# Kernel optimization log

Measured on AMD Instinct MI355X. Metric: run time of the kernel, lower is better.

The kernel has to match this reference:

```python
import jax, jax.numpy as jnp
import numpy as np

GROUP = 64   # quantization group size (nunchaku W4A4 default)
QMAX = 7.0   # symmetric int4 positive range


def setup_inputs() -> dict:
    key = jax.random.key(0)
    ks = jax.random.split(key, 6)
    T, K, N, R = 256, 3072, 3072, 32
    x = jax.random.normal(ks[0], (T, K), dtype=jnp.float32)
    # int4 weight codes stored as 0..15 (dequant subtracts zero-point 8)
    qweight = jax.random.randint(ks[1], (N, K), 0, 16, dtype=jnp.int32)
    # per-(out_channel, input_group) weight scales, small positive
    wscales = jax.random.uniform(ks[2], (N, K // GROUP), dtype=jnp.float32) * 0.02 + 1e-3
    lora_down = jax.random.normal(ks[3], (R, K), dtype=jnp.float32) / np.sqrt(K)
    lora_up = jax.random.normal(ks[4], (N, R), dtype=jnp.float32) / np.sqrt(R)
    bias = jax.random.normal(ks[5], (N,), dtype=jnp.float32) * 0.01
    return {"x": x, "qweight": qweight, "wscales": wscales,
            "lora_down": lora_down, "lora_up": lora_up, "bias": bias}


def _quantize_act(x):
    # per-token, per-group symmetric int4 fake-quant (quantize -> dequantize)
    T, K = x.shape
    xg = x.reshape(T, K // GROUP, GROUP)
    scale = jnp.maximum(jnp.max(jnp.abs(xg), axis=-1, keepdims=True) / QMAX, 1e-8)
    q = jnp.clip(jnp.round(xg / scale), -8.0, QMAX)
    return (q * scale).reshape(T, K)


def reference(x, qweight, wscales, lora_down, lora_up, bias):
    # Dequantize int4 weights: (code - 8) * per-group scale  -> [N, K]
    N, K = qweight.shape
    w = (qweight.astype(jnp.float32) - 8.0).reshape(N, K // GROUP, GROUP)
    w = (w * wscales[:, :, None]).reshape(N, K)
    # W4A4 main path: int4-quantized activations x dequantized int4 weights
    x_dq = _quantize_act(x)
    main = x_dq @ w.T                               # [T, N]
    # fused low-rank (SVDQuant LoRA) branch on full-precision activations
    lora = (x @ lora_down.T) @ lora_up.T            # [T, R] @ [R, N]
    return main + lora + bias
```

## Files before the change

kernel.cpp:

```cpp
#include <hip/hip_runtime.h>
#include <stdint.h>

#define T_DIM 256
#define K_DIM 3072
#define N_DIM 3072
#define R_DIM 32
#define KG    48
#define NSPLIT 6

#define PQ_BLOCKS 4608
#define QA_BLOCKS 3072
#define LM_BLOCKS 96
#define BO_BLOCKS 768

typedef __bf16 bf16x8 __attribute__((ext_vector_type(8)));
typedef float  f32x4  __attribute__((ext_vector_type(4)));
typedef unsigned short u16x8 __attribute__((ext_vector_type(8)));

__device__ __forceinline__ unsigned short f2bf(float f) {
    unsigned u = __builtin_bit_cast(unsigned, f);
    unsigned rounding = 0x7FFFu + ((u >> 16) & 1u);
    return (unsigned short)((u + rounding) >> 16);
}

__device__ __forceinline__ bf16x8 cvt8(const float* p) {
    float4 lo = ((const float4*)p)[0], hi = ((const float4*)p)[1];
    bf16x8 v;
    v[0] = (__bf16)lo.x; v[1] = (__bf16)lo.y; v[2] = (__bf16)lo.z; v[3] = (__bf16)lo.w;
    v[4] = (__bf16)hi.x; v[5] = (__bf16)hi.y; v[6] = (__bf16)hi.z; v[7] = (__bf16)hi.w;
    return v;
}

__global__ __launch_bounds__(256) void prep(
        const int*   __restrict__ qweight,
        const float* __restrict__ x,
        const float* __restrict__ lora_down,
        const float* __restrict__ bias,
        unsigned*       __restrict__ Qp,
        unsigned short* __restrict__ Ap,
        float*          __restrict__ Lm,
        float*          __restrict__ out) {
    int blk = blockIdx.x;
    if (blk < PQ_BLOCKS) {
        size_t o = (size_t)blk * 256 + threadIdx.x;
        unsigned kt  = (unsigned)(o / 24576u);
        unsigned rem = (unsigned)(o % 24576u);
        unsigned n = rem >> 3, wi = rem & 7;
        const int4* p = (const int4*)(qweight + (size_t)n * K_DIM + (size_t)kt * 64 + wi * 8);
        int4 a = p[0], b = p[1];
        unsigned w = (unsigned)(a.x & 15)        | ((unsigned)(a.y & 15) << 4)
                   | ((unsigned)(a.z & 15) << 8) | ((unsigned)(a.w & 15) << 12)
                   | ((unsigned)(b.x & 15) << 16)| ((unsigned)(b.y & 15) << 20)
                   | ((unsigned)(b.z & 15) << 24)| ((unsigned)(b.w & 15) << 28);
        Qp[o] = w;
    } else if (blk < PQ_BLOCKS + QA_BLOCKS) {
        int widx = (blk - PQ_BLOCKS) * 4 + (threadIdx.x >> 6);
        int lane = threadIdx.x & 63;
        int t = widx / KG, g = widx % KG;
        float v = x[(size_t)t * K_DIM + g * 64 + lane];
        float a = fabsf(v);
        #pragma unroll
        for (int off = 32; off; off >>= 1) a = fmaxf(a, __shfl_xor(a, off));
        float scale = fmaxf(a / 7.0f, 1e-8f);
        float q = rintf(v / scale);
        q = fminf(fmaxf(q, -8.f), 7.f);
        Ap[(((size_t)g * 8 + (lane >> 3)) * 256 + t) * 8 + (lane & 7)] = f2bf(q * scale);
    } else if (blk < PQ_BLOCKS + QA_BLOCKS + LM_BLOCKS) {
        int kb = blk - PQ_BLOCKS - QA_BLOCKS;
        int lane = threadIdx.x & 63, wv = threadIdx.x >> 6;
        int mrow = lane & 15, quad = lane >> 4;
        int k0 = kb * 32 + quad * 8;
        bf16x8 a[4], b[2];
        #pragma unroll
        for (int mt = 0; mt < 4; ++mt)
            a[mt] = cvt8(x + (size_t)(wv * 64 + mt * 16 + mrow) * K_DIM + k0);
        #pragma unroll
        for (int nt = 0; nt < 2; ++nt)
            b[nt] = cvt8(lora_down + (size_t)(nt * 16 + mrow) * K_DIM + k0);
        f32x4 acc[4][2];
        f32x4 zero = {0.f, 0.f, 0.f, 0.f};
        #pragma unroll
        for (int i = 0; i < 4; ++i) { acc[i][0] = zero; acc[i][1] = zero; }
        #pragma unroll
        for (int mt = 0; mt < 4; ++mt)
            #pragma unroll
            for (int nt = 0; nt < 2; ++nt)
                acc[mt][nt] = __builtin_amdgcn_mfma_f32_16x16x32_bf16(
                    a[mt], b[nt], acc[mt][nt], 0, 0, 0);
        #pragma unroll
        for (int mt = 0; mt < 4; ++mt)
            #pragma unroll
            for (int nt = 0; nt < 2; ++nt)
                #pragma unroll
                for (int r = 0; r < 4; ++r)
                    atomicAdd(&Lm[(size_t)(wv * 64 + mt * 16 + quad * 4 + r) * R_DIM
                                  + nt * 16 + mrow], acc[mt][nt][r]);
    } else {
        int i = (blk - PQ_BLOCKS - QA_BLOCKS - LM_BLOCKS) * 256 + threadIdx.x;
        float4 bv = *(const float4*)&bias[(i * 4) % N_DIM];
        ((float4*)out)[i] = bv;
    }
}

__global__ __launch_bounds__(256) void gemm_main(
        const uint4*    __restrict__ ApU,
        const unsigned* __restrict__ Qp,
        const float*    __restrict__ wscales,
        const float*    __restrict__ Lm,
        const float*    __restrict__ lora_up,
        float*          __restrict__ out) {
    __shared__ uint4 BsU[2][512];
    int nblk  = blockIdx.x;
    int mblk  = blockIdx.y;
    int split = blockIdx.z;
    int c0 = split * (KG / NSPLIT);
    int c1 = (split == NSPLIT - 1) ? KG + 1 : c0 + (KG / NSPLIT);
    int tid = threadIdx.x;
    int lane = tid & 63, wv = tid >> 6;
    int mrow = lane & 15, quad = lane >> 4;
    int n_row = tid >> 2, seg = tid & 3;
    const int nbase = nblk * 64;
    const int mbase = mblk * 128 + wv * 32;

    f32x4 acc[2][4];
    f32x4 zero = {0.f, 0.f, 0.f, 0.f};
    #pragma unroll
    for (int i = 0; i < 2; ++i)
        #pragma unroll
        for (int j = 0; j < 4; ++j) acc[i][j] = zero;

    uint2 ubc[2];
    float wsr[2];
    bf16x8 af[2][2][2];

    const float* wsrow = wscales + (size_t)(nbase + n_row) * KG;

    #define AFRAG(kt, ks, mt) \
        (*(const bf16x8*)&ApU[(size_t)(kt) * 2048 + ((ks) * 4 + quad) * 256 + \
                              mbase + (mt) * 16 + mrow])

    {
        #pragma unroll
        for (int ks = 0; ks < 2; ++ks)
            #pragma unroll
            for (int mt = 0; mt < 2; ++mt)
                af[0][ks][mt] = AFRAG(c0, ks, mt);
        const unsigned* q0 = Qp + ((size_t)c0 * N_DIM + nbase + n_row) * 8 + seg * 2;
        const unsigned* q1 = Qp + ((size_t)(c0 + 1) * N_DIM + nbase + n_row) * 8 + seg * 2;
        ubc[0] = *(const uint2*)q0;
        ubc[1] = *(const uint2*)q1;
        wsr[0] = wsrow[c0];
        wsr[1] = wsrow[c0 + 1];
    }

    #define STEP(PP, KT)                                                          \
    {                                                                             \
        constexpr int p = (PP);                                                   \
        const int kk = (KT);                                                      \
        if (kk < KG) {                                                            \
            float w = wsr[p];                                                     \
            float m8w = -8.0f * w;                                                \
            unsigned u0 = ubc[p].x, u1 = ubc[p].y;                                \
            unsigned e0 = u0 & 0x0F0F0F0Fu, od0 = (u0 >> 4) & 0x0F0F0F0Fu;        \
            unsigned e1 = u1 & 0x0F0F0F0Fu, od1 = (u1 >> 4) & 0x0F0F0F0Fu;        \
            bf16x8 v0, v1;                                                        \
            _Pragma("unroll")                                                     \
            for (int j = 0; j < 4; ++j) {                                         \
                v0[2*j]   = (__bf16)__builtin_fmaf((float)((e0  >> (8*j)) & 0xFFu), w, m8w); \
                v0[2*j+1] = (__bf16)__builtin_fmaf((float)((od0 >> (8*j)) & 0xFFu), w, m8w); \
                v1[2*j]   = (__bf16)__builtin_fmaf((float)((e1  >> (8*j)) & 0xFFu), w, m8w); \
                v1[2*j+1] = (__bf16)__builtin_fmaf((float)((od1 >> (8*j)) & 0xFFu), w, m8w); \
            }                                                                     \
            BsU[p][(seg * 2 + 0) * 64 + n_row] = __builtin_bit_cast(uint4, v0);   \
            BsU[p][(seg * 2 + 1) * 64 + n_row] = __builtin_bit_cast(uint4, v1);   \
        } else {                                                                  \
            bf16x8 v0 = __builtin_bit_cast(bf16x8, (u16x8)(0));                   \
            bf16x8 v1 = __builtin_bit_cast(bf16x8, (u16x8)(0));                   \
            if (seg < 2) {                                                        \
                const float* lu = lora_up + (size_t)(nbase + n_row) * R_DIM + seg * 16; \
                _Pragma("unroll")                                                 \
                for (int j = 0; j < 8; ++j) {                                     \
                    v0[j] = (__bf16)lu[j];                                        \
                    v1[j] = (__bf16)lu[8 + j];                                    \
                }                                                                 \
            }                                                                     \
            BsU[p][(seg * 2 + 0) * 64 + n_row] = __builtin_bit_cast(uint4, v0);   \
            BsU[p][(seg * 2 + 1) * 64 + n_row] = __builtin_bit_cast(uint4, v1);   \
        }                                                                         \
        __syncthreads();                                                          \
        if (kk + 2 < c1 && kk + 2 < KG) {                                         \
            const unsigned* q2 = Qp + ((size_t)(kk + 2) * N_DIM + nbase + n_row) * 8 + seg * 2; \
            ubc[p] = *(const uint2*)q2;                                           \
            wsr[p] = wsrow[kk + 2];                                               \
        }                                                                         \
        if (kk + 1 < c1) {                                                        \
            if (kk + 1 < KG) {                                                    \
                _Pragma("unroll")                                                 \
                for (int ks = 0; ks < 2; ++ks)                                    \
                    _Pragma("unroll")                                             \
                    for (int mt = 0; mt < 2; ++mt)                                \
                        af[p ^ 1][ks][mt] = AFRAG(kk + 1, ks, mt);                \
            } else {                                                              \
                _Pragma("unroll")                                                 \
                for (int mt = 0; mt < 2; ++mt) {                                  \
                    int row = mbase + mt * 16 + mrow;                             \
                    if (quad < 4)                                                 \
                        af[p ^ 1][0][mt] = cvt8(Lm + (size_t)row * R_DIM + quad * 8); \
                    else                                                          \
                        af[p ^ 1][0][mt] = __builtin_bit_cast(bf16x8, (u16x8)(0)); \
                    af[p ^ 1][1][mt] = __builtin_bit_cast(bf16x8, (u16x8)(0));    \
                }                                                                 \
            }                                                                     \
        }                                                                         \
        _Pragma("unroll")                                                         \
        for (int ks = 0; ks < 2; ++ks) {                                          \
            bf16x8 b[4];                                                          \
            _Pragma("unroll")                                                     \
            for (int nt = 0; nt < 4; ++nt) {                                      \
                uint4 tb = BsU[p][(ks * 4 + quad) * 64 + nt * 16 + mrow];         \
                b[nt] = __builtin_bit_cast(bf16x8, tb);                           \
            }                                                                     \
            _Pragma("unroll")                                                     \
            for (int mt = 0; mt < 2; ++mt)                                        \
                _Pragma("unroll")                                                 \
                for (int nt = 0; nt < 4; ++nt)                                    \
                    acc[mt][nt] = __builtin_amdgcn_mfma_f32_16x16x32_bf16(        \
                        af[p][ks][mt], b[nt], acc[mt][nt], 0, 0, 0);              \
        }                                                                         \
    }

    int kt = c0;
    for (; kt + 1 < c1; kt += 2) {
        STEP(0, kt);
        STEP(1, kt + 1);
    }
    if (kt < c1) STEP(0, kt);

    #undef STEP
    #undef AFRAG
    #pragma unroll
    for (int nt = 0; nt < 4; ++nt) {
        int n = nbase + nt * 16 + mrow;
        #pragma unroll
        for (int mt = 0; mt < 2; ++mt) {
            int row0 = mblk * 128 + wv * 32 + mt * 16 + quad * 4;
            #pragma unroll
            for (int r = 0; r < 4; ++r)
                atomicAdd(&out[(size_t)(row0 + r) * N_DIM + n], acc[mt][nt][r]);
        }
    }
}

extern "C" void kernel_launch(void* const* d_in, const int* in_sizes, int n_in,
                              void* d_out, int out_size, void* d_ws, size_t ws_size,
                              hipStream_t stream) {
    const float* x         = (const float*)d_in[0];
    const int*   qweight   = (const int*)d_in[1];
    const float* wscales   = (const float*)d_in[2];
    const float* lora_down = (const float*)d_in[3];
    const float* lora_up   = (const float*)d_in[4];
    const float* bias      = (const float*)d_in[5];

    char* wsp = (char*)d_ws;
    unsigned short* Ap = (unsigned short*)wsp;
    wsp += (size_t)KG * 2048 * 16;
    float* Lm = (float*)wsp;
    wsp += (size_t)T_DIM * R_DIM * 4;
    unsigned* Qp = (unsigned*)wsp;

    hipMemsetAsync(Lm, 0, (size_t)T_DIM * R_DIM * sizeof(float), stream);
    prep<<<PQ_BLOCKS + QA_BLOCKS + LM_BLOCKS + BO_BLOCKS, 256, 0, stream>>>(
        qweight, x, lora_down, bias, Qp, Ap, Lm, (float*)d_out);
    gemm_main<<<dim3(48, 2, NSPLIT), 256, 0, stream>>>(
        (const uint4*)Ap, Qp, wscales, Lm, lora_up, (float*)d_out);
}
```

Before: 119.3 us.

## Fuse prep and GEMM into one persistent kernel with grid barriers

Merges the prep kernel (weight packing, activation quantization, bias init, LoRA-down) and the main GEMM into a single 576-block launch. Grid-wide spin barriers separate the phases, and the prep work is spread across blocks with strided loops. The Lm memset is folded into the kernel, so only a small barrier memset is still launched. This removes a kernel launch and the inter-kernel gap, but the barrier only works if all 576 blocks are co-resident, and it has a timeout escape that could silently break ordering.

```diff
diff --git a/kernel.cpp b/kernel.cpp
--- a/kernel.cpp
+++ b/kernel.cpp
@@ -8,10 +8,7 @@
 #define KG    48
 #define NSPLIT 6
 
-#define PQ_BLOCKS 4608
-#define QA_BLOCKS 3072
-#define LM_BLOCKS 96
-#define BO_BLOCKS 768
+#define GRID_BLOCKS 576
 
 typedef __bf16 bf16x8 __attribute__((ext_vector_type(8)));
 typedef float  f32x4  __attribute__((ext_vector_type(4)));
@@ -31,43 +28,80 @@
     return v;
 }
 
-__global__ __launch_bounds__(256) void prep(
+__device__ __forceinline__ void grid_barrier(unsigned* cell) {
+    __syncthreads();
+    if (threadIdx.x == 0) {
+        __hip_atomic_fetch_add(cell, 1u, __ATOMIC_RELEASE, __HIP_MEMORY_SCOPE_AGENT);
+        unsigned long long t0 = __builtin_amdgcn_s_memrealtime();
+        while (__hip_atomic_load(cell, __ATOMIC_ACQUIRE, __HIP_MEMORY_SCOPE_AGENT)
+               < (unsigned)GRID_BLOCKS) {
+            __builtin_amdgcn_s_sleep(8);
+            if (__builtin_amdgcn_s_memrealtime() - t0 > (1ULL << 24)) break;
+        }
+    }
+    __syncthreads();
+}
+
+__global__ __launch_bounds__(256, 3) void fused(
+        const float* __restrict__ x,
         const int*   __restrict__ qweight,
-        const float* __restrict__ x,
+        const float* __restrict__ wscales,
         const float* __restrict__ lora_down,
+        const float* __restrict__ lora_up,
         const float* __restrict__ bias,
         unsigned*       __restrict__ Qp,
         unsigned short* __restrict__ Ap,
         float*          __restrict__ Lm,
+        unsigned*       __restrict__ bar,
         float*          __restrict__ out) {
-    int blk = blockIdx.x;
-    if (blk < PQ_BLOCKS) {
-        size_t o = (size_t)blk * 256 + threadIdx.x;
-        unsigned kt  = (unsigned)(o / 24576u);
-        unsigned rem = (unsigned)(o % 24576u);
-        unsigned n = rem >> 3, wi = rem & 7;
-        const int4* p = (const int4*)(qweight + (size_t)n * K_DIM + (size_t)kt * 64 + wi * 8);
-        int4 a = p[0], b = p[1];
-        unsigned w = (unsigned)(a.x & 15)        | ((unsigned)(a.y & 15) << 4)
-                   | ((unsigned)(a.z & 15) << 8) | ((unsigned)(a.w & 15) << 12)
-                   | ((unsigned)(b.x & 15) << 16)| ((unsigned)(b.y & 15) << 20)
-                   | ((unsigned)(b.z & 15) << 24)| ((unsigned)(b.w & 15) << 28);
-        Qp[o] = w;
-    } else if (blk < PQ_BLOCKS + QA_BLOCKS) {
-        int widx = (blk - PQ_BLOCKS) * 4 + (threadIdx.x >> 6);
-        int lane = threadIdx.x & 63;
-        int t = widx / KG, g = widx % KG;
-        float v = x[(size_t)t * K_DIM + g * 64 + lane];
-        float a = fabsf(v);
-        #pragma unroll
-        for (int off = 32; off; off >>= 1) a = fmaxf(a, __shfl_xor(a, off));
-        float scale = fmaxf(a / 7.0f, 1e-8f);
-        float q = rintf(v / scale);
-        q = fminf(fmaxf(q, -8.f), 7.f);
-        Ap[(((size_t)g * 8 + (lane >> 3)) * 256 + t) * 8 + (lane & 7)] = f2bf(q * scale);
-    } else if (blk < PQ_BLOCKS + QA_BLOCKS + LM_BLOCKS) {
-        int kb = blk - PQ_BLOCKS - QA_BLOCKS;
-        int lane = threadIdx.x & 63, wv = threadIdx.x >> 6;
+    __shared__ uint4 BsU[2][512];
+    const int blk = blockIdx.x;
+    const int tid = threadIdx.x;
+
+    {
+        #pragma unroll
+        for (int i = 0; i < 8; ++i) {
+            size_t o = ((size_t)blk * 8 + i) * 256 + tid;
+            unsigned kt  = (unsigned)(o / 24576u);
+            unsigned rem = (unsigned)(o % 24576u);
+            unsigned n = rem >> 3, wi = rem & 7;
+            const int4* p = (const int4*)(qweight + (size_t)n * K_DIM + (size_t)kt * 64 + wi * 8);
+            int4 a = p[0], b = p[1];
+            unsigned w = (unsigned)(a.x & 15)        | ((unsigned)(a.y & 15) << 4)
+                       | ((unsigned)(a.z & 15) << 8) | ((unsigned)(a.w & 15) << 12)
+                       | ((unsigned)(b.x & 15) << 16)| ((unsigned)(b.y & 15) << 20)
+                       | ((unsigned)(b.z & 15) << 24)| ((unsigned)(b.w & 15) << 28);
+            Qp[o] = w;
+        }
+    }
+    {
+        int lane = tid & 63;
+        int wgl  = blk * 4 + (tid >> 6);
+        for (int u = wgl; u < T_DIM * KG; u += GRID_BLOCKS * 4) {
+            int t = u / KG, g = u % KG;
+            float v = x[(size_t)t * K_DIM + g * 64 + lane];
+            float a = fabsf(v);
+            #pragma unroll
+            for (int off = 32; off; off >>= 1) a = fmaxf(a, __shfl_xor(a, off));
+            float scale = fmaxf(a / 7.0f, 1e-8f);
+            float q = rintf(v / scale);
+            q = fminf(fmaxf(q, -8.f), 7.f);
+            Ap[(((size_t)g * 8 + (lane >> 3)) * 256 + t) * 8 + (lane & 7)] = f2bf(q * scale);
+        }
+    }
+    {
+        for (int u = blk * 256 + tid; u < T_DIM * N_DIM / 4; u += GRID_BLOCKS * 256) {
+            float4 bv = *(const float4*)&bias[(u * 4) % N_DIM];
+            ((float4*)out)[u] = bv;
+        }
+    }
+    if (blk < 32) Lm[blk * 256 + tid] = 0.f;
+
+    grid_barrier(&bar[0]);
+
+    if (blk < 96) {
+        int kb = blk;
+        int lane = tid & 63, wv = tid >> 6;
         int mrow = lane & 15, quad = lane >> 4;
         int k0 = kb * 32 + quad * 8;
         bf16x8 a[4], b[2];
@@ -95,158 +129,151 @@
                 for (int r = 0; r < 4; ++r)
                     atomicAdd(&Lm[(size_t)(wv * 64 + mt * 16 + quad * 4 + r) * R_DIM
                                   + nt * 16 + mrow], acc[mt][nt][r]);
-    } else {
-        int i = (blk - PQ_BLOCKS - QA_BLOCKS - LM_BLOCKS) * 256 + threadIdx.x;
-        float4 bv = *(const float4*)&bias[(i * 4) % N_DIM];
-        ((float4*)out)[i] = bv;
-    }
-}
-
-__global__ __launch_bounds__(256) void gemm_main(
-        const uint4*    __restrict__ ApU,
-        const unsigned* __restrict__ Qp,
-        const float*    __restrict__ wscales,
-        const float*    __restrict__ Lm,
-        const float*    __restrict__ lora_up,
-        float*          __restrict__ out) {
-    __shared__ uint4 BsU[2][512];
-    int nblk  = blockIdx.x;
-    int mblk  = blockIdx.y;
-    int split = blockIdx.z;
-    int c0 = split * (KG / NSPLIT);
-    int c1 = (split == NSPLIT - 1) ? KG + 1 : c0 + (KG / NSPLIT);
-    int tid = threadIdx.x;
-    int lane = tid & 63, wv = tid >> 6;
-    int mrow = lane & 15, quad = lane >> 4;
-    int n_row = tid >> 2, seg = tid & 3;
-    const int nbase = nblk * 64;
-    const int mbase = mblk * 128 + wv * 32;
-
-    f32x4 acc[2][4];
-    f32x4 zero = {0.f, 0.f, 0.f, 0.f};
-    #pragma unroll
-    for (int i = 0; i < 2; ++i)
-        #pragma unroll
-        for (int j = 0; j < 4; ++j) acc[i][j] = zero;
-
-    uint2 ubc[2];
-    float wsr[2];
-    bf16x8 af[2][2][2];
-
-    const float* wsrow = wscales + (size_t)(nbase + n_row) * KG;
-
-    #define AFRAG(kt, ks, mt) \
-        (*(const bf16x8*)&ApU[(size_t)(kt) * 2048 + ((ks) * 4 + quad) * 256 + \
-                              mbase + (mt) * 16 + mrow])
+    }
+
+    grid_barrier(&bar[1]);
 
     {
-        #pragma unroll
-        for (int ks = 0; ks < 2; ++ks)
-            #pragma unroll
-            for (int mt = 0; mt < 2; ++mt)
-                af[0][ks][mt] = AFRAG(c0, ks, mt);
-        const unsigned* q0 = Qp + ((size_t)c0 * N_DIM + nbase + n_row) * 8 + seg * 2;
-        const unsigned* q1 = Qp + ((size_t)(c0 + 1) * N_DIM + nbase + n_row) * 8 + seg * 2;
-        ubc[0] = *(const uint2*)q0;
-        ubc[1] = *(const uint2*)q1;
-        wsr[0] = wsrow[c0];
-        wsr[1] = wsrow[c0 + 1];
-    }
-
-    #define STEP(PP, KT)                                                          \
-    {                                                                             \
-        constexpr int p = (PP);                                                   \
-        const int kk = (KT);                                                      \
-        if (kk < KG) {                                                            \
-            float w = wsr[p];                                                     \
-            float m8w = -8.0f * w;                                                \
-            unsigned u0 = ubc[p].x, u1 = ubc[p].y;                                \
-            unsigned e0 = u0 & 0x0F0F0F0Fu, od0 = (u0 >> 4) & 0x0F0F0F0Fu;        \
-            unsigned e1 = u1 & 0x0F0F0F0Fu, od1 = (u1 >> 4) & 0x0F0F0F0Fu;        \
-            bf16x8 v0, v1;                                                        \
-            _Pragma("unroll")                                                     \
-            for (int j = 0; j < 4; ++j) {                                         \
-                v0[2*j]   = (__bf16)__builtin_fmaf((float)((e0  >> (8*j)) & 0xFFu), w, m8w); \
-                v0[2*j+1] = (__bf16)__builtin_fmaf((float)((od0 >> (8*j)) & 0xFFu), w, m8w); \
-                v1[2*j]   = (__bf16)__builtin_fmaf((float)((e1  >> (8*j)) & 0xFFu), w, m8w); \
-                v1[2*j+1] = (__bf16)__builtin_fmaf((float)((od1 >> (8*j)) & 0xFFu), w, m8w); \
-            }                                                                     \
-            BsU[p][(seg * 2 + 0) * 64 + n_row] = __builtin_bit_cast(uint4, v0);   \
-            BsU[p][(seg * 2 + 1) * 64 + n_row] = __builtin_bit_cast(uint4, v1);   \
-        } else {                                                                  \
-            bf16x8 v0 = __builtin_bit_cast(bf16x8, (u16x8)(0));                   \
-            bf16x8 v1 = __builtin_bit_cast(bf16x8, (u16x8)(0));                   \
-            if (seg < 2) {                                                        \
-                const float* lu = lora_up + (size_t)(nbase + n_row) * R_DIM + seg * 16; \
-                _Pragma("unroll")                                                 \
-                for (int j = 0; j < 8; ++j) {                                     \
-                    v0[j] = (__bf16)lu[j];                                        \
-                    v1[j] = (__bf16)lu[8 + j];                                    \
-                }                                                                 \
-            }                                                                     \
-            BsU[p][(seg * 2 + 0) * 64 + n_row] = __builtin_bit_cast(uint4, v0);   \
-            BsU[p][(seg * 2 + 1) * 64 + n_row] = __builtin_bit_cast(uint4, v1);   \
-        }                                                                         \
-        __syncthreads();                                                          \
-        if (kk + 2 < c1 && kk + 2 < KG) {                                         \
-            const unsigned* q2 = Qp + ((size_t)(kk + 2) * N_DIM + nbase + n_row) * 8 + seg * 2; \
-            ubc[p] = *(const uint2*)q2;                                           \
-            wsr[p] = wsrow[kk + 2];                                               \
-        }                                                                         \
-        if (kk + 1 < c1) {                                                        \
-            if (kk + 1 < KG) {                                                    \
-                _Pragma("unroll")                                                 \
-                for (int ks = 0; ks < 2; ++ks)                                    \
-                    _Pragma("unroll")                                             \
-                    for (int mt = 0; mt < 2; ++mt)                                \
-                        af[p ^ 1][ks][mt] = AFRAG(kk + 1, ks, mt);                \
-            } else {                                                              \
-                _Pragma("unroll")                                                 \
-                for (int mt = 0; mt < 2; ++mt) {                                  \
-                    int row = mbase + mt * 16 + mrow;                             \
-                    if (quad < 4)                                                 \
-                        af[p ^ 1][0][mt] = cvt8(Lm + (size_t)row * R_DIM + quad * 8); \
-                    else                                                          \
-                        af[p ^ 1][0][mt] = __builtin_bit_cast(bf16x8, (u16x8)(0)); \
-                    af[p ^ 1][1][mt] = __builtin_bit_cast(bf16x8, (u16x8)(0));    \
-                }                                                                 \
-            }                                                                     \
-        }                                                                         \
-        _Pragma("unroll")                                                         \
-        for (int ks = 0; ks < 2; ++ks) {                                          \
-            bf16x8 b[4];                                                          \
-            _Pragma("unroll")                                                     \
-            for (int nt = 0; nt < 4; ++nt) {                                      \
-                uint4 tb = BsU[p][(ks * 4 + quad) * 64 + nt * 16 + mrow];         \
-                b[nt] = __builtin_bit_cast(bf16x8, tb);                           \
-            }                                                                     \
-            _Pragma("unroll")                                                     \
-            for (int mt = 0; mt < 2; ++mt)                                        \
-                _Pragma("unroll")                                                 \
-                for (int nt = 0; nt < 4; ++nt)                                    \
-                    acc[mt][nt] = __builtin_amdgcn_mfma_f32_16x16x32_bf16(        \
-                        af[p][ks][mt], b[nt], acc[mt][nt], 0, 0, 0);              \
-        }                                                                         \
-    }
-
-    int kt = c0;
-    for (; kt + 1 < c1; kt += 2) {
-        STEP(0, kt);
-        STEP(1, kt + 1);
-    }
-    if (kt < c1) STEP(0, kt);
-
-    #undef STEP
-    #undef AFRAG
-    #pragma unroll
-    for (int nt = 0; nt < 4; ++nt) {
-        int n = nbase + nt * 16 + mrow;
-        #pragma unroll
-        for (int mt = 0; mt < 2; ++mt) {
-            int row0 = mblk * 128 + wv * 32 + mt * 16 + quad * 4;
-            #pragma unroll
-            for (int r = 0; r < 4; ++r)
-                atomicAdd(&out[(size_t)(row0 + r) * N_DIM + n], acc[mt][nt][r]);
+        const uint4* ApU = (const uint4*)Ap;
+        int split = blk / 96;
+        int rem   = blk % 96;
+        int nblk  = rem % 48;
+        int mblk  = rem / 48;
+        int c0 = split * (KG / NSPLIT);
+        int c1 = (split == NSPLIT - 1) ? KG + 1 : c0 + (KG / NSPLIT);
+        int lane = tid & 63, wv = tid >> 6;
+        int mrow = lane & 15, quad = lane >> 4;
+        int n_row = tid >> 2, seg = tid & 3;
+        const int nbase = nblk * 64;
+        const int mbase = mblk * 128 + wv * 32;
+
+        f32x4 acc[2][4];
+        f32x4 zero = {0.f, 0.f, 0.f, 0.f};
+        #pragma unroll
+        for (int i = 0; i < 2; ++i)
+            #pragma unroll
+            for (int j = 0; j < 4; ++j) acc[i][j] = zero;
+
+        uint2 ubc[2];
+        float wsr[2];
+        bf16x8 af[2][2][2];
+
+        const float* wsrow = wscales + (size_t)(nbase + n_row) * KG;
+
+        #define AFRAG(kt, ks, mt) \
+            (*(const bf16x8*)&ApU[(size_t)(kt) * 2048 + ((ks) * 4 + quad) * 256 + \
+                                  mbase + (mt) * 16 + mrow])
+
+        {
+            #pragma unroll
+            for (int ks = 0; ks < 2; ++ks)
+                #pragma unroll
+                for (int mt = 0; mt < 2; ++mt)
+                    af[0][ks][mt] = AFRAG(c0, ks, mt);
+            const unsigned* q0 = Qp + ((size_t)c0 * N_DIM + nbase + n_row) * 8 + seg * 2;
+            const unsigned* q1 = Qp + ((size_t)(c0 + 1) * N_DIM + nbase + n_row) * 8 + seg * 2;
+            ubc[0] = *(const uint2*)q0;
+            ubc[1] = *(const uint2*)q1;
+            wsr[0] = wsrow[c0];
+            wsr[1] = wsrow[c0 + 1];
+        }
+
+        #define STEP(PP, KT)                                                          \
+        {                                                                             \
+            constexpr int p = (PP);                                                   \
+            const int kk = (KT);                                                      \
+            if (kk < KG) {                                                            \
+                float w = wsr[p];                                                     \
+                float m8w = -8.0f * w;                                                \
+                unsigned u0 = ubc[p].x, u1 = ubc[p].y;                                \
+                unsigned e0 = u0 & 0x0F0F0F0Fu, od0 = (u0 >> 4) & 0x0F0F0F0Fu;        \
+                unsigned e1 = u1 & 0x0F0F0F0Fu, od1 = (u1 >> 4) & 0x0F0F0F0Fu;        \
+                bf16x8 v0, v1;                                                        \
+                _Pragma("unroll")                                                     \
+                for (int j = 0; j < 4; ++j) {                                         \
+                    v0[2*j]   = (__bf16)__builtin_fmaf((float)((e0  >> (8*j)) & 0xFFu), w, m8w); \
+                    v0[2*j+1] = (__bf16)__builtin_fmaf((float)((od0 >> (8*j)) & 0xFFu), w, m8w); \
+                    v1[2*j]   = (__bf16)__builtin_fmaf((float)((e1  >> (8*j)) & 0xFFu), w, m8w); \
+                    v1[2*j+1] = (__bf16)__builtin_fmaf((float)((od1 >> (8*j)) & 0xFFu), w, m8w); \
+                }                                                                     \
+                BsU[p][(seg * 2 + 0) * 64 + n_row] = __builtin_bit_cast(uint4, v0);   \
+                BsU[p][(seg * 2 + 1) * 64 + n_row] = __builtin_bit_cast(uint4, v1);   \
+            } else {                                                                  \
+                bf16x8 v0 = __builtin_bit_cast(bf16x8, (u16x8)(0));                   \
+                bf16x8 v1 = __builtin_bit_cast(bf16x8, (u16x8)(0));                   \
+                if (seg < 2) {                                                        \
+                    const float* lu = lora_up + (size_t)(nbase + n_row) * R_DIM + seg * 16; \
+                    _Pragma("unroll")                                                 \
+                    for (int j = 0; j < 8; ++j) {                                     \
+                        v0[j] = (__bf16)lu[j];                                        \
+                        v1[j] = (__bf16)lu[8 + j];                                    \
+                    }                                                                 \
+                }                                                                     \
+                BsU[p][(seg * 2 + 0) * 64 + n_row] = __builtin_bit_cast(uint4, v0);   \
+                BsU[p][(seg * 2 + 1) * 64 + n_row] = __builtin_bit_cast(uint4, v1);   \
+            }                                                                         \
+            __syncthreads();                                                          \
+            if (kk + 2 < c1 && kk + 2 < KG) {                                         \
+                const unsigned* q2 = Qp + ((size_t)(kk + 2) * N_DIM + nbase + n_row) * 8 + seg * 2; \
+                ubc[p] = *(const uint2*)q2;                                           \
+                wsr[p] = wsrow[kk + 2];                                               \
+            }                                                                         \
+            if (kk + 1 < c1) {                                                        \
+                if (kk + 1 < KG) {                                                    \
+                    _Pragma("unroll")                                                 \
+                    for (int ks = 0; ks < 2; ++ks)                                    \
+                        _Pragma("unroll")                                             \
+                        for (int mt = 0; mt < 2; ++mt)                                \
+                            af[p ^ 1][ks][mt] = AFRAG(kk + 1, ks, mt);                \
+                } else {                                                              \
+                    _Pragma("unroll")                                                 \
+                    for (int mt = 0; mt < 2; ++mt) {                                  \
+                        int row = mbase + mt * 16 + mrow;                             \
+                        if (quad < 4)                                                 \
+                            af[p ^ 1][0][mt] = cvt8(Lm + (size_t)row * R_DIM + quad * 8); \
+                        else                                                          \
+                            af[p ^ 1][0][mt] = __builtin_bit_cast(bf16x8, (u16x8)(0)); \
+                        af[p ^ 1][1][mt] = __builtin_bit_cast(bf16x8, (u16x8)(0));    \
+                    }                                                                 \
+                }                                                                     \
+            }                                                                         \
+            _Pragma("unroll")                                                         \
+            for (int ks = 0; ks < 2; ++ks) {                                          \
+                bf16x8 b[4];                                                          \
+                _Pragma("unroll")                                                     \
+                for (int nt = 0; nt < 4; ++nt) {                                      \
+                    uint4 tb = BsU[p][(ks * 4 + quad) * 64 + nt * 16 + mrow];         \
+                    b[nt] = __builtin_bit_cast(bf16x8, tb);                           \
+                }                                                                     \
+                _Pragma("unroll")                                                     \
+                for (int mt = 0; mt < 2; ++mt)                                        \
+                    _Pragma("unroll")                                                 \
+                    for (int nt = 0; nt < 4; ++nt)                                    \
+                        acc[mt][nt] = __builtin_amdgcn_mfma_f32_16x16x32_bf16(        \
+                            af[p][ks][mt], b[nt], acc[mt][nt], 0, 0, 0);              \
+            }                                                                         \
+        }
+
+        int kt = c0;
+        for (; kt + 1 < c1; kt += 2) {
+            STEP(0, kt);
+            STEP(1, kt + 1);
+        }
+        if (kt < c1) STEP(0, kt);
+
+        #undef STEP
+        #undef AFRAG
+
+        #pragma unroll
+        for (int nt = 0; nt < 4; ++nt) {
+            int n = nbase + nt * 16 + mrow;
+            #pragma unroll
+            for (int mt = 0; mt < 2; ++mt) {
+                int row0 = mblk * 128 + wv * 32 + mt * 16 + quad * 4;
+                #pragma unroll
+                for (int r = 0; r < 4; ++r)
+                    atomicAdd(&out[(size_t)(row0 + r) * N_DIM + n], acc[mt][nt][r]);
+            }
         }
     }
 }
@@ -267,10 +294,11 @@
     float* Lm = (float*)wsp;
     wsp += (size_t)T_DIM * R_DIM * 4;
     unsigned* Qp = (unsigned*)wsp;
-
-    hipMemsetAsync(Lm, 0, (size_t)T_DIM * R_DIM * sizeof(float), stream);
-    prep<<<PQ_BLOCKS + QA_BLOCKS + LM_BLOCKS + BO_BLOCKS, 256, 0, stream>>>(
-        qweight, x, lora_down, bias, Qp, Ap, Lm, (float*)d_out);
-    gemm_main<<<dim3(48, 2, NSPLIT), 256, 0, stream>>>(
-        (const uint4*)Ap, Qp, wscales, Lm, lora_up, (float*)d_out);
-}
+    wsp += (size_t)N_DIM * (K_DIM / 8) * 4;
+    unsigned* bar = (unsigned*)wsp;
+
+    hipMemsetAsync(bar, 0, 64, stream);
+    fused<<<GRID_BLOCKS, 256, 0, stream>>>(
+        x, qweight, wscales, lora_down, lora_up, bias,
+        Qp, Ap, Lm, bar, (float*)d_out);
+}
```

Measured after the change: 252.8 us. 2.12x slower.

## Dequantize raw int32 weight codes directly in GEMM, dropping the nibble-packing pre-pass

Applied to the files above, without the earlier changes.

The prep kernel no longer repacks int32 weight codes into 4-bit nibbles in a workspace buffer. The main GEMM now loads the raw int32 codes straight from qweight (four int4 vectors per thread per k-tile), converts each code to float and applies the group scale while staging into shared memory. This removes one full pass over the weights and the write-then-read of the packed buffer. In exchange, the GEMM streams the full 32-bit codes, and each weight row is fetched by both M blocks. It also holds many more registers for the prefetched codes, which may lower occupancy.

```diff
diff --git a/kernel.cpp b/kernel.cpp
--- a/kernel.cpp
+++ b/kernel.cpp
@@ -8,7 +8,6 @@
 #define KG    48
 #define NSPLIT 6
 
-#define PQ_BLOCKS 4608
 #define QA_BLOCKS 3072
 #define LM_BLOCKS 96
 #define BO_BLOCKS 768
@@ -32,29 +31,15 @@
 }
 
 __global__ __launch_bounds__(256) void prep(
-        const int*   __restrict__ qweight,
         const float* __restrict__ x,
         const float* __restrict__ lora_down,
         const float* __restrict__ bias,
-        unsigned*       __restrict__ Qp,
         unsigned short* __restrict__ Ap,
         float*          __restrict__ Lm,
         float*          __restrict__ out) {
     int blk = blockIdx.x;
-    if (blk < PQ_BLOCKS) {
-        size_t o = (size_t)blk * 256 + threadIdx.x;
-        unsigned kt  = (unsigned)(o / 24576u);
-        unsigned rem = (unsigned)(o % 24576u);
-        unsigned n = rem >> 3, wi = rem & 7;
-        const int4* p = (const int4*)(qweight + (size_t)n * K_DIM + (size_t)kt * 64 + wi * 8);
-        int4 a = p[0], b = p[1];
-        unsigned w = (unsigned)(a.x & 15)        | ((unsigned)(a.y & 15) << 4)
-                   | ((unsigned)(a.z & 15) << 8) | ((unsigned)(a.w & 15) << 12)
-                   | ((unsigned)(b.x & 15) << 16)| ((unsigned)(b.y & 15) << 20)
-                   | ((unsigned)(b.z & 15) << 24)| ((unsigned)(b.w & 15) << 28);
-        Qp[o] = w;
-    } else if (blk < PQ_BLOCKS + QA_BLOCKS) {
-        int widx = (blk - PQ_BLOCKS) * 4 + (threadIdx.x >> 6);
+    if (blk < QA_BLOCKS) {
+        int widx = blk * 4 + (threadIdx.x >> 6);
         int lane = threadIdx.x & 63;
         int t = widx / KG, g = widx % KG;
         float v = x[(size_t)t * K_DIM + g * 64 + lane];
@@ -65,8 +50,8 @@
         float q = rintf(v / scale);
         q = fminf(fmaxf(q, -8.f), 7.f);
         Ap[(((size_t)g * 8 + (lane >> 3)) * 256 + t) * 8 + (lane & 7)] = f2bf(q * scale);
-    } else if (blk < PQ_BLOCKS + QA_BLOCKS + LM_BLOCKS) {
-        int kb = blk - PQ_BLOCKS - QA_BLOCKS;
+    } else if (blk < QA_BLOCKS + LM_BLOCKS) {
+        int kb = blk - QA_BLOCKS;
         int lane = threadIdx.x & 63, wv = threadIdx.x >> 6;
         int mrow = lane & 15, quad = lane >> 4;
         int k0 = kb * 32 + quad * 8;
@@ -96,7 +81,7 @@
                     atomicAdd(&Lm[(size_t)(wv * 64 + mt * 16 + quad * 4 + r) * R_DIM
                                   + nt * 16 + mrow], acc[mt][nt][r]);
     } else {
-        int i = (blk - PQ_BLOCKS - QA_BLOCKS - LM_BLOCKS) * 256 + threadIdx.x;
+        int i = (blk - QA_BLOCKS - LM_BLOCKS) * 256 + threadIdx.x;
         float4 bv = *(const float4*)&bias[(i * 4) % N_DIM];
         ((float4*)out)[i] = bv;
     }
@@ -104,7 +89,7 @@
 
 __global__ __launch_bounds__(256) void gemm_main(
         const uint4*    __restrict__ ApU,
-        const unsigned* __restrict__ Qp,
+        const int*      __restrict__ qweight,
         const float*    __restrict__ wscales,
         const float*    __restrict__ Lm,
         const float*    __restrict__ lora_up,
@@ -129,11 +114,12 @@
         #pragma unroll
         for (int j = 0; j < 4; ++j) acc[i][j] = zero;
 
-    uint2 ubc[2];
+    int4  qc[2][4];
     float wsr[2];
     bf16x8 af[2][2][2];
 
     const float* wsrow = wscales + (size_t)(nbase + n_row) * KG;
+    const int4* qrow = (const int4*)(qweight + (size_t)(nbase + n_row) * K_DIM + seg * 16);
 
     #define AFRAG(kt, ks, mt) \
         (*(const bf16x8*)&ApU[(size_t)(kt) * 2048 + ((ks) * 4 + quad) * 256 + \
@@ -145,10 +131,11 @@
             #pragma unroll
             for (int mt = 0; mt < 2; ++mt)
                 af[0][ks][mt] = AFRAG(c0, ks, mt);
-        const unsigned* q0 = Qp + ((size_t)c0 * N_DIM + nbase + n_row) * 8 + seg * 2;
-        const unsigned* q1 = Qp + ((size_t)(c0 + 1) * N_DIM + nbase + n_row) * 8 + seg * 2;
-        ubc[0] = *(const uint2*)q0;
-        ubc[1] = *(const uint2*)q1;
+        #pragma unroll
+        for (int j = 0; j < 4; ++j) {
+            qc[0][j] = qrow[(size_t)c0 * 16 + j];
+            qc[1][j] = qrow[(size_t)(c0 + 1) * 16 + j];
+        }
         wsr[0] = wsrow[c0];
         wsr[1] = wsrow[c0 + 1];
     }
@@ -160,17 +147,24 @@
         if (kk < KG) {                                                            \
             float w = wsr[p];                                                     \
             float m8w = -8.0f * w;                                                \
-            unsigned u0 = ubc[p].x, u1 = ubc[p].y;                                \
-            unsigned e0 = u0 & 0x0F0F0F0Fu, od0 = (u0 >> 4) & 0x0F0F0F0Fu;        \
-            unsigned e1 = u1 & 0x0F0F0F0Fu, od1 = (u1 >> 4) & 0x0F0F0F0Fu;        \
+            int4 ca = qc[p][0], cb = qc[p][1], cc = qc[p][2], cd = qc[p][3];      \
             bf16x8 v0, v1;                                                        \
-            _Pragma("unroll")                                                     \
-            for (int j = 0; j < 4; ++j) {                                         \
-                v0[2*j]   = (__bf16)__builtin_fmaf((float)((e0  >> (8*j)) & 0xFFu), w, m8w); \
-                v0[2*j+1] = (__bf16)__builtin_fmaf((float)((od0 >> (8*j)) & 0xFFu), w, m8w); \
-                v1[2*j]   = (__bf16)__builtin_fmaf((float)((e1  >> (8*j)) & 0xFFu), w, m8w); \
-                v1[2*j+1] = (__bf16)__builtin_fmaf((float)((od1 >> (8*j)) & 0xFFu), w, m8w); \
-            }                                                                     \
+            v0[0] = (__bf16)__builtin_fmaf((float)ca.x, w, m8w);                  \
+            v0[1] = (__bf16)__builtin_fmaf((float)ca.y, w, m8w);                  \
+            v0[2] = (__bf16)__builtin_fmaf((float)ca.z, w, m8w);                  \
+            v0[3] = (__bf16)__builtin_fmaf((float)ca.w, w, m8w);                  \
+            v0[4] = (__bf16)__builtin_fmaf((float)cb.x, w, m8w);                  \
+            v0[5] = (__bf16)__builtin_fmaf((float)cb.y, w, m8w);                  \
+            v0[6] = (__bf16)__builtin_fmaf((float)cb.z, w, m8w);                  \
+            v0[7] = (__bf16)__builtin_fmaf((float)cb.w, w, m8w);                  \
+            v1[0] = (__bf16)__builtin_fmaf((float)cc.x, w, m8w);                  \
+            v1[1] = (__bf16)__builtin_fmaf((float)cc.y, w, m8w);                  \
+            v1[2] = (__bf16)__builtin_fmaf((float)cc.z, w, m8w);                  \
+            v1[3] = (__bf16)__builtin_fmaf((float)cc.w, w, m8w);                  \
+            v1[4] = (__bf16)__builtin_fmaf((float)cd.x, w, m8w);                  \
+            v1[5] = (__bf16)__builtin_fmaf((float)cd.y, w, m8w);                  \
+            v1[6] = (__bf16)__builtin_fmaf((float)cd.z, w, m8w);                  \
+            v1[7] = (__bf16)__builtin_fmaf((float)cd.w, w, m8w);                  \
             BsU[p][(seg * 2 + 0) * 64 + n_row] = __builtin_bit_cast(uint4, v0);   \
             BsU[p][(seg * 2 + 1) * 64 + n_row] = __builtin_bit_cast(uint4, v1);   \
         } else {                                                                  \
@@ -189,8 +183,9 @@
         }                                                                         \
         __syncthreads();                                                          \
         if (kk + 2 < c1 && kk + 2 < KG) {                                         \
-            const unsigned* q2 = Qp + ((size_t)(kk + 2) * N_DIM + nbase + n_row) * 8 + seg * 2; \
-            ubc[p] = *(const uint2*)q2;                                           \
+            _Pragma("unroll")                                                     \
+            for (int j = 0; j < 4; ++j)                                           \
+                qc[p][j] = qrow[(size_t)(kk + 2) * 16 + j];                       \
             wsr[p] = wsrow[kk + 2];                                               \
         }                                                                         \
         if (kk + 1 < c1) {                                                        \
@@ -265,12 +260,10 @@
     unsigned short* Ap = (unsigned short*)wsp;
     wsp += (size_t)KG * 2048 * 16;
     float* Lm = (float*)wsp;
-    wsp += (size_t)T_DIM * R_DIM * 4;
-    unsigned* Qp = (unsigned*)wsp;
 
     hipMemsetAsync(Lm, 0, (size_t)T_DIM * R_DIM * sizeof(float), stream);
-    prep<<<PQ_BLOCKS + QA_BLOCKS + LM_BLOCKS + BO_BLOCKS, 256, 0, stream>>>(
-        qweight, x, lora_down, bias, Qp, Ap, Lm, (float*)d_out);
+    prep<<<QA_BLOCKS + LM_BLOCKS + BO_BLOCKS, 256, 0, stream>>>(
+        x, lora_down, bias, Ap, Lm, (float*)d_out);
     gemm_main<<<dim3(48, 2, NSPLIT), 256, 0, stream>>>(
-        (const uint4*)Ap, Qp, wscales, Lm, lora_up, (float*)d_out);
-}
+        (const uint4*)Ap, qweight, wscales, Lm, lora_up, (float*)d_out);
+}
```

After: 116.5 us. -2.3%, faster.
